# Kernel tuning notes

Measured on AMD Instinct MI355X. Metric: run time of the kernel, lower is better.

Reference implementation:

```python
import jax, jax.numpy as jnp
import numpy as np

N = 50000   # nodes per graph
D = 256     # embedding dim
E = 800000  # edges per graph
NEG_SLOPE = 0.2
EPS = 1e-9


def gat_layer(h, src, dst, W, a):
    # SpGraphAttentionLayer: transform, edge attention exp(-leakyrelu(a.[h_i||h_j])),
    # softmax-normalized scatter aggregation, ELU activation.
    h = h @ W                                   # [N, D]
    # a.[h_src || h_dst] == (h @ a[:D])[src] + (h @ a[D:])[dst]  (avoids [E,2D] concat)
    alpha_src = h @ a[:D]                       # [N]
    alpha_dst = h @ a[D:]                       # [N]
    logits = alpha_src[src] + alpha_dst[dst]    # [E]
    e = jnp.exp(-jax.nn.leaky_relu(logits, NEG_SLOPE))  # [E], pyGAT sparse form
    rowsum = jax.ops.segment_sum(e, src, num_segments=N)            # [N]
    num = jax.ops.segment_sum(e[:, None] * h[dst], src, num_segments=N)  # [N, D]
    out = num / (rowsum[:, None] + EPS)
    return jax.nn.elu(out)


def setup_inputs() -> dict:
    key = jax.random.key(0)
    ks = jax.random.split(key, 8)
    w_std = float(np.sqrt(2.0 / (D + D)))  # xavier
    sr_emb = jax.random.normal(ks[0], (N, D), jnp.float32) * w_std
    tg_emb = jax.random.normal(ks[1], (N, D), jnp.float32) * w_std
    W1 = jax.random.normal(ks[2], (D, D), jnp.float32) * w_std
    a1 = jax.random.normal(ks[3], (2 * D,), jnp.float32) * 0.1
    W2 = jax.random.normal(ks[4], (D, D), jnp.float32) * w_std
    a2 = jax.random.normal(ks[5], (2 * D,), jnp.float32) * 0.1
    adj_sr = jax.random.randint(ks[6], (2, E), 0, N, dtype=jnp.int64)
    adj_tg = jax.random.randint(ks[7], (2, E), 0, N, dtype=jnp.int64)
    return {"sr_emb": sr_emb, "tg_emb": tg_emb, "W1": W1, "a1": a1,
            "W2": W2, "a2": a2, "adj_sr": adj_sr, "adj_tg": adj_tg}


def reference(sr_emb, tg_emb, W1, a1, W2, a2, adj_sr, adj_tg):
    # layers are shared across the two graphs (same ModuleList applied to both)
    src_s, dst_s = adj_sr[0], adj_sr[1]
    src_t, dst_t = adj_tg[0], adj_tg[1]
    for (W, a) in ((W1, a1), (W2, a2)):
        sr_emb = gat_layer(sr_emb, src_s, dst_s, W, a)
        tg_emb = gat_layer(tg_emb, src_t, dst_t, W, a)
    return (sr_emb, tg_emb)
```

## Files before the change

### kernel.cpp

```cpp
#include <hip/hip_runtime.h>

#define NEG_SLOPE 0.2f
#define EPS_ 1e-9f

typedef __attribute__((ext_vector_type(8))) short short8v;
typedef __attribute__((ext_vector_type(4))) float f32x4;

__device__ __forceinline__ float bf2f(unsigned short u) {
    return __uint_as_float(((unsigned)u) << 16);
}
__device__ __forceinline__ unsigned short f2bf(float f) {
    unsigned u = __float_as_uint(f);
    u = u + 0x7FFFu + ((u >> 16) & 1u);
    return (unsigned short)(u >> 16);
}

__global__ void hist_kernel(const int* __restrict__ src, int* __restrict__ cnt, int E) {
    int i = blockIdx.x * blockDim.x + threadIdx.x;
    if (i < E) atomicAdd(&cnt[src[i]], 1);
}

__global__ __launch_bounds__(256) void scan1_kernel(const int* __restrict__ cnt,
        int* __restrict__ locpre, int* __restrict__ blocksum, int n) {
    int t = threadIdx.x;
    int lane = t & 63, wid = t >> 6;
    int base = blockIdx.x * 1024 + t * 4;
    int4 v = {0, 0, 0, 0};
    if (base + 3 < n) {
        v = *(const int4*)(cnt + base);
    } else {
        if (base + 0 < n) v.x = cnt[base + 0];
        if (base + 1 < n) v.y = cnt[base + 1];
        if (base + 2 < n) v.z = cnt[base + 2];
        if (base + 3 < n) v.w = cnt[base + 3];
    }
    int s = v.x + v.y + v.z + v.w;
    int incl = s;
    for (int off = 1; off < 64; off <<= 1) {
        int u = __shfl_up(incl, off);
        if (lane >= off) incl += u;
    }
    __shared__ int ws[4];
    if (lane == 63) ws[wid] = incl;
    __syncthreads();
    int woff = 0;
    for (int i = 0; i < wid; ++i) woff += ws[i];
    int excl = incl - s + woff;
    int4 o;
    o.x = excl; o.y = excl + v.x; o.z = o.y + v.y; o.w = o.z + v.z;
    if (base + 3 < n) {
        *(int4*)(locpre + base) = o;
    } else {
        if (base + 0 < n) locpre[base + 0] = o.x;
        if (base + 1 < n) locpre[base + 1] = o.y;
        if (base + 2 < n) locpre[base + 2] = o.z;
        if (base + 3 < n) locpre[base + 3] = o.w;
    }
    if (t == 255) blocksum[blockIdx.x] = excl + s;
}

__global__ __launch_bounds__(64) void scan2_kernel(int* __restrict__ blocksum, int nb) {
    int lane = threadIdx.x;
    int carry = 0;
    for (int base = 0; base < nb; base += 64) {
        int v = (base + lane < nb) ? blocksum[base + lane] : 0;
        int incl = v;
        for (int off = 1; off < 64; off <<= 1) {
            int u = __shfl_up(incl, off);
            if (lane >= off) incl += u;
        }
        int tot = __shfl(incl, 63);
        if (base + lane < nb) blocksum[base + lane] = incl - v + carry;
        carry += tot;
    }
}

__global__ __launch_bounds__(256) void scan3_kernel(const int* __restrict__ locpre,
        const int* __restrict__ blocksum, int* __restrict__ row_ptr,
        int* __restrict__ cursor, int n, int total) {
    int base = blockIdx.x * 1024 + threadIdx.x * 4;
    int off = blocksum[blockIdx.x];
    if (base + 3 < n) {
        int4 v = *(const int4*)(locpre + base);
        v.x += off; v.y += off; v.z += off; v.w += off;
        *(int4*)(row_ptr + base) = v;
        *(int4*)(cursor + base) = v;
    } else {
        for (int i = 0; i < 4; ++i) {
            if (base + i < n) {
                int v = locpre[base + i] + off;
                row_ptr[base + i] = v;
                cursor[base + i] = v;
            }
        }
    }
    if (blockIdx.x == 0 && threadIdx.x == 0) row_ptr[n] = total;
}

__global__ void scatter_kernel(const int* __restrict__ src, const int* __restrict__ dst,
        int* __restrict__ cursor, int* __restrict__ colv, int E) {
    int i = blockIdx.x * blockDim.x + threadIdx.x;
    if (i < E) {
        int p = atomicAdd(&cursor[src[i]], 1);
        colv[p] = dst[i];
    }
}

__global__ void wt_kernel(const float* __restrict__ W, short* __restrict__ Wt) {
    int nn = blockIdx.x, k = threadIdx.x;
    Wt[nn * 256 + k] = (short)f2bf(W[k * 256 + nn]);
}

template<bool IN_BF16>
__global__ __launch_bounds__(256) void gemm_kernel(const void* __restrict__ hin,
        const short* __restrict__ Wt, short* __restrict__ hp,
        const float* __restrict__ af, float* __restrict__ asrc,
        float* __restrict__ adst, int M) {
    __shared__ short As[64 * 40];
    __shared__ short Bt[256 * 40];
    int tid = threadIdx.x;
    int lane = tid & 63, w = tid >> 6;
    int m0 = blockIdx.x * 64;

    f32x4 acc[16];
#pragma unroll
    for (int t = 0; t < 16; ++t) acc[t] = (f32x4){0.f, 0.f, 0.f, 0.f};

    int ar = tid >> 2;
    int ac = (tid & 3) * 8;
    int agrow = m0 + ar;

    for (int kk = 0; kk < 256; kk += 32) {
        short8v av = (short8v){0,0,0,0,0,0,0,0};
        if constexpr (IN_BF16) {
            if (agrow < M)
                av = *(const short8v*)((const short*)hin + (size_t)agrow * 256 + kk + ac);
        } else {
            if (agrow < M) {
                const float* s = (const float*)hin + (size_t)agrow * 256 + kk + ac;
                float4 v0 = *(const float4*)s;
                float4 v1 = *(const float4*)(s + 4);
                av[0] = (short)f2bf(v0.x); av[1] = (short)f2bf(v0.y);
                av[2] = (short)f2bf(v0.z); av[3] = (short)f2bf(v0.w);
                av[4] = (short)f2bf(v1.x); av[5] = (short)f2bf(v1.y);
                av[6] = (short)f2bf(v1.z); av[7] = (short)f2bf(v1.w);
            }
        }
        *(short8v*)&As[ar * 40 + ac] = av;
        {
            const short* s = Wt + (size_t)tid * 256 + kk;
#pragma unroll
            for (int i = 0; i < 4; ++i)
                *(short8v*)&Bt[tid * 40 + i * 8] = *(const short8v*)(s + i * 8);
        }
        __syncthreads();
        short8v a = *(const short8v*)&As[(16 * w + (lane & 15)) * 40 + (lane >> 4) * 8];
#pragma unroll
        for (int t = 0; t < 16; ++t) {
            short8v b = *(const short8v*)&Bt[(16 * t + (lane & 15)) * 40 + (lane >> 4) * 8];
            acc[t] = __builtin_amdgcn_mfma_f32_16x16x32_bf16(a, b, acc[t], 0, 0, 0);
        }
        __syncthreads();
    }
    int r0 = 16 * w + (lane >> 4) * 4;
    int c0 = lane & 15;
    float a_s[16], a_d[16];
#pragma unroll
    for (int t = 0; t < 16; ++t) {
        a_s[t] = af[16 * t + c0];
        a_d[t] = af[256 + 16 * t + c0];
    }
#pragma unroll
    for (int j = 0; j < 4; ++j) {
        int grow = m0 + r0 + j;
        float ssrc = 0.f, sdst = 0.f;
#pragma unroll
        for (int t = 0; t < 16; ++t) {
            float cv = acc[t][j];
            ssrc = fmaf(cv, a_s[t], ssrc);
            sdst = fmaf(cv, a_d[t], sdst);
            if (grow < M) hp[(size_t)grow * 256 + 16 * t + c0] = (short)f2bf(cv);
        }
        for (int off = 1; off < 16; off <<= 1) {
            ssrc += __shfl_xor(ssrc, off);
            sdst += __shfl_xor(sdst, off);
        }
        if (c0 == 0 && grow < M) { asrc[grow] = ssrc; adst[grow] = sdst; }
    }
}

template<bool OUT_BF16>
__global__ __launch_bounds__(256) void aggregate_kernel(const int* __restrict__ row_ptr,
        const int* __restrict__ colv, const float* __restrict__ asrc,
        const float* __restrict__ adst, const unsigned short* __restrict__ hp,
        void* __restrict__ outp, int n) {
    int node = (blockIdx.x * blockDim.x + threadIdx.x) >> 6;
    int lane = threadIdx.x & 63;
    if (node >= n) return;
    node = __builtin_amdgcn_readfirstlane(node);
    int beg = row_ptr[node], end = row_ptr[node + 1];
    float ai = asrc[node];
    const ushort4* __restrict__ hpv = (const ushort4*)hp;
    float acc0 = 0.f, acc1 = 0.f, acc2 = 0.f, acc3 = 0.f, rs = 0.f;
    for (int e = beg; e < end; e += 16) {
        int m = end - e;
        int js[16]; float ds[16]; ushort4 qs[16];
#pragma unroll
        for (int k = 0; k < 16; ++k)
            if (k < m) { js[k] = colv[e + k]; ds[k] = adst[js[k]]; }
#pragma unroll
        for (int k = 0; k < 16; ++k)
            if (k < m) qs[k] = hpv[(size_t)js[k] * 64 + lane];
#pragma unroll
        for (int k = 0; k < 16; ++k)
            if (k < m) {
                float x = ai + ds[k];
                float lr = fmaxf(x, NEG_SLOPE * x);
                float wk = __expf(-lr);
                ushort4 q = qs[k];
                acc0 = fmaf(wk, bf2f(q.x), acc0);
                acc1 = fmaf(wk, bf2f(q.y), acc1);
                acc2 = fmaf(wk, bf2f(q.z), acc2);
                acc3 = fmaf(wk, bf2f(q.w), acc3);
                rs += wk;
            }
    }
    float inv = 1.f / (rs + EPS_);
    float v0 = acc0 * inv, v1 = acc1 * inv, v2 = acc2 * inv, v3 = acc3 * inv;
    v0 = v0 > 0.f ? v0 : __expf(v0) - 1.f;
    v1 = v1 > 0.f ? v1 : __expf(v1) - 1.f;
    v2 = v2 > 0.f ? v2 : __expf(v2) - 1.f;
    v3 = v3 > 0.f ? v3 : __expf(v3) - 1.f;
    if constexpr (OUT_BF16) {
        ushort4 o;
        o.x = f2bf(v0); o.y = f2bf(v1); o.z = f2bf(v2); o.w = f2bf(v3);
        *(ushort4*)((unsigned short*)outp + (size_t)node * 256 + lane * 4) = o;
    } else {
        float4 o = {v0, v1, v2, v3};
        *(float4*)((float*)outp + (size_t)node * 256 + lane * 4) = o;
    }
}

extern "C" void kernel_launch(void* const* d_in, const int* in_sizes, int n_in,
                              void* d_out, int out_size, void* d_ws, size_t ws_size,
                              hipStream_t stream) {
    const float* sr_emb = (const float*)d_in[0];
    const float* tg_emb = (const float*)d_in[1];
    const float* W1 = (const float*)d_in[2];
    const float* a1 = (const float*)d_in[3];
    const float* W2 = (const float*)d_in[4];
    const float* a2 = (const float*)d_in[5];
    const int* adj_sr = (const int*)d_in[6];
    const int* adj_tg = (const int*)d_in[7];
    int N = in_sizes[0] / 256;
    int E = in_sizes[6] / 2;

    char* p = (char*)d_ws;
    auto alloc = [&](size_t bytes) -> void* {
        void* r = (void*)p;
        p += (bytes + 255) & ~(size_t)255;
        return r;
    };
    int nb = (N + 1023) / 1024;
    int* cnt      = (int*)alloc((size_t)N * 4);
    int* row_ptr  = (int*)alloc((size_t)(N + 1) * 4);
    int* cursor   = (int*)alloc((size_t)N * 4);
    int* locpre   = (int*)alloc((size_t)N * 4);
    int* blocksum = (int*)alloc((size_t)nb * 4);
    int* colv     = (int*)alloc((size_t)E * 4);
    short* Wt1    = (short*)alloc(256 * 256 * 2);
    short* Wt2    = (short*)alloc(256 * 256 * 2);
    short* hp     = (short*)alloc((size_t)N * 256 * 2);
    float* asrc   = (float*)alloc((size_t)N * 4);
    float* adst   = (float*)alloc((size_t)N * 4);
    short* tmp    = (short*)alloc((size_t)N * 256 * 2);

    wt_kernel<<<256, 256, 0, stream>>>(W1, Wt1);
    wt_kernel<<<256, 256, 0, stream>>>(W2, Wt2);

    int gemm_grid = (N + 63) / 64;
    int nw_grid = (N + 3) / 4;
    int e_grid = (E + 255) / 256;

    for (int g = 0; g < 2; ++g) {
        const int* srcv = (g == 0 ? adj_sr : adj_tg);
        const int* dstv = srcv + E;
        const float* emb = (g == 0 ? sr_emb : tg_emb);
        float* outg = (float*)d_out + (size_t)g * N * 256;

        hipMemsetAsync(cnt, 0, (size_t)N * 4, stream);
        hist_kernel<<<e_grid, 256, 0, stream>>>(srcv, cnt, E);
        scan1_kernel<<<nb, 256, 0, stream>>>(cnt, locpre, blocksum, N);
        scan2_kernel<<<1, 64, 0, stream>>>(blocksum, nb);
        scan3_kernel<<<nb, 256, 0, stream>>>(locpre, blocksum, row_ptr, cursor, N, E);
        scatter_kernel<<<e_grid, 256, 0, stream>>>(srcv, dstv, cursor, colv, E);

        gemm_kernel<false><<<gemm_grid, 256, 0, stream>>>(emb, Wt1, hp, a1, asrc, adst, N);
        aggregate_kernel<true><<<nw_grid, 256, 0, stream>>>(row_ptr, colv, asrc, adst,
                (const unsigned short*)hp, tmp, N);
        gemm_kernel<true><<<gemm_grid, 256, 0, stream>>>(tmp, Wt2, hp, a2, asrc, adst, N);
        aggregate_kernel<false><<<nw_grid, 256, 0, stream>>>(row_ptr, colv, asrc, adst,
                (const unsigned short*)hp, outg, N);
    }
}
```

Baseline: 716.4 us.

## Precompute edge attention weights in a separate kernel and vectorize aggregation loads

```diff
diff --git a/kernel.cpp b/kernel.cpp
--- a/kernel.cpp
+++ b/kernel.cpp
@@ -98,11 +98,24 @@
 }
 
 __global__ void scatter_kernel(const int* __restrict__ src, const int* __restrict__ dst,
-        int* __restrict__ cursor, int* __restrict__ colv, int E) {
+        int* __restrict__ cursor, int* __restrict__ colv, int* __restrict__ srce, int E) {
     int i = blockIdx.x * blockDim.x + threadIdx.x;
     if (i < E) {
-        int p = atomicAdd(&cursor[src[i]], 1);
+        int s = src[i];
+        int p = atomicAdd(&cursor[s], 1);
         colv[p] = dst[i];
+        srce[p] = s;
+    }
+}
+
+__global__ __launch_bounds__(256) void ew_kernel(const int* __restrict__ srce,
+        const int* __restrict__ colv, const float* __restrict__ asrc,
+        const float* __restrict__ adst, float* __restrict__ ew, int E) {
+    int i = blockIdx.x * blockDim.x + threadIdx.x;
+    if (i < E) {
+        float x = asrc[srce[i]] + adst[colv[i]];
+        float lr = fmaxf(x, NEG_SLOPE * x);
+        ew[i] = __expf(-lr);
     }
 }
 
@@ -189,41 +202,71 @@
     }
 }
 
+#define GATH(qq, jj) qq = hpv[(size_t)(jj) * 64 + lane];
+#define CONS(qq, ww) { acc0 = fmaf(ww, bf2f(qq.x), acc0); acc1 = fmaf(ww, bf2f(qq.y), acc1); \
+                       acc2 = fmaf(ww, bf2f(qq.z), acc2); acc3 = fmaf(ww, bf2f(qq.w), acc3); \
+                       rs += ww; }
+
 template<bool OUT_BF16>
 __global__ __launch_bounds__(256) void aggregate_kernel(const int* __restrict__ row_ptr,
-        const int* __restrict__ colv, const float* __restrict__ asrc,
-        const float* __restrict__ adst, const unsigned short* __restrict__ hp,
-        void* __restrict__ outp, int n) {
+        const int* __restrict__ colv, const float* __restrict__ ew,
+        const unsigned short* __restrict__ hp, void* __restrict__ outp, int n) {
     int node = (blockIdx.x * blockDim.x + threadIdx.x) >> 6;
     int lane = threadIdx.x & 63;
     if (node >= n) return;
-    node = __builtin_amdgcn_readfirstlane(node);
     int beg = row_ptr[node], end = row_ptr[node + 1];
-    float ai = asrc[node];
     const ushort4* __restrict__ hpv = (const ushort4*)hp;
     float acc0 = 0.f, acc1 = 0.f, acc2 = 0.f, acc3 = 0.f, rs = 0.f;
-    for (int e = beg; e < end; e += 16) {
+    int e = beg;
+    for (; e + 16 <= end; e += 16) {
+        int4 j0 = *(const int4*)(colv + e);
+        int4 j1 = *(const int4*)(colv + e + 4);
+        int4 j2 = *(const int4*)(colv + e + 8);
+        int4 j3 = *(const int4*)(colv + e + 12);
+        float4 w0 = *(const float4*)(ew + e);
+        float4 w1 = *(const float4*)(ew + e + 4);
+        float4 w2 = *(const float4*)(ew + e + 8);
+        float4 w3 = *(const float4*)(ew + e + 12);
+        ushort4 q0, q1, q2, q3, q4, q5, q6, q7, q8, q9, qa, qb, qc, qd, qe, qf;
+        GATH(q0, j0.x) GATH(q1, j0.y) GATH(q2, j0.z) GATH(q3, j0.w)
+        GATH(q4, j1.x) GATH(q5, j1.y) GATH(q6, j1.z) GATH(q7, j1.w)
+        GATH(q8, j2.x) GATH(q9, j2.y) GATH(qa, j2.z) GATH(qb, j2.w)
+        GATH(qc, j3.x) GATH(qd, j3.y) GATH(qe, j3.z) GATH(qf, j3.w)
+        CONS(q0, w0.x) CONS(q1, w0.y) CONS(q2, w0.z) CONS(q3, w0.w)
+        CONS(q4, w1.x) CONS(q5, w1.y) CONS(q6, w1.z) CONS(q7, w1.w)
+        CONS(q8, w2.x) CONS(q9, w2.y) CONS(qa, w2.z) CONS(qb, w2.w)
+        CONS(qc, w3.x) CONS(qd, w3.y) CONS(qe, w3.z) CONS(qf, w3.w)
+    }
+    if (e < end) {
         int m = end - e;
-        int js[16]; float ds[16]; ushort4 qs[16];
-#pragma unroll
-        for (int k = 0; k < 16; ++k)
-            if (k < m) { js[k] = colv[e + k]; ds[k] = adst[js[k]]; }
-#pragma unroll
-        for (int k = 0; k < 16; ++k)
-            if (k < m) qs[k] = hpv[(size_t)js[k] * 64 + lane];
-#pragma unroll
-        for (int k = 0; k < 16; ++k)
-            if (k < m) {
-                float x = ai + ds[k];
-                float lr = fmaxf(x, NEG_SLOPE * x);
-                float wk = __expf(-lr);
-                ushort4 q = qs[k];
-                acc0 = fmaf(wk, bf2f(q.x), acc0);
-                acc1 = fmaf(wk, bf2f(q.y), acc1);
-                acc2 = fmaf(wk, bf2f(q.z), acc2);
-                acc3 = fmaf(wk, bf2f(q.w), acc3);
-                rs += wk;
-            }
+        int4 j0 = *(const int4*)(colv + e);
+        int4 j1 = *(const int4*)(colv + e + 4);
+        int4 j2 = *(const int4*)(colv + e + 8);
+        int4 j3 = *(const int4*)(colv + e + 12);
+        float4 w0 = *(const float4*)(ew + e);
+        float4 w1 = *(const float4*)(ew + e + 4);
+        float4 w2 = *(const float4*)(ew + e + 8);
+        float4 w3 = *(const float4*)(ew + e + 12);
+        ushort4 q0, q1, q2, q3, q4, q5, q6, q7, q8, q9, qa, qb, qc, qd, qe, qf;
+        GATH(q0, j0.x) GATH(q1, j0.y) GATH(q2, j0.z) GATH(q3, j0.w)
+        GATH(q4, j1.x) GATH(q5, j1.y) GATH(q6, j1.z) GATH(q7, j1.w)
+        GATH(q8, j2.x) GATH(q9, j2.y) GATH(qa, j2.z) GATH(qb, j2.w)
+        GATH(qc, j3.x) GATH(qd, j3.y) GATH(qe, j3.z) GATH(qf, j3.w)
+        CONS(q0, w0.x)
+        if (m > 1)  CONS(q1, w0.y)
+        if (m > 2)  CONS(q2, w0.z)
+        if (m > 3)  CONS(q3, w0.w)
+        if (m > 4)  CONS(q4, w1.x)
+        if (m > 5)  CONS(q5, w1.y)
+        if (m > 6)  CONS(q6, w1.z)
+        if (m > 7)  CONS(q7, w1.w)
+        if (m > 8)  CONS(q8, w2.x)
+        if (m > 9)  CONS(q9, w2.y)
+        if (m > 10) CONS(qa, w2.z)
+        if (m > 11) CONS(qb, w2.w)
+        if (m > 12) CONS(qc, w3.x)
+        if (m > 13) CONS(qd, w3.y)
+        if (m > 14) CONS(qe, w3.z)
     }
     float inv = 1.f / (rs + EPS_);
     float v0 = acc0 * inv, v1 = acc1 * inv, v2 = acc2 * inv, v3 = acc3 * inv;
@@ -267,7 +310,9 @@
     int* cursor   = (int*)alloc((size_t)N * 4);
     int* locpre   = (int*)alloc((size_t)N * 4);
     int* blocksum = (int*)alloc((size_t)nb * 4);
-    int* colv     = (int*)alloc((size_t)E * 4);
+    int* colv     = (int*)alloc((size_t)(E + 16) * 4);
+    int* srce     = (int*)alloc((size_t)E * 4);
+    float* ew     = (float*)alloc((size_t)(E + 16) * 4);
     short* Wt1    = (short*)alloc(256 * 256 * 2);
     short* Wt2    = (short*)alloc(256 * 256 * 2);
     short* hp     = (short*)alloc((size_t)N * 256 * 2);
@@ -289,17 +334,20 @@
         float* outg = (float*)d_out + (size_t)g * N * 256;
 
         hipMemsetAsync(cnt, 0, (size_t)N * 4, stream);
+        hipMemsetAsync(colv + E, 0, 16 * 4, stream);
         hist_kernel<<<e_grid, 256, 0, stream>>>(srcv, cnt, E);
         scan1_kernel<<<nb, 256, 0, stream>>>(cnt, locpre, blocksum, N);
         scan2_kernel<<<1, 64, 0, stream>>>(blocksum, nb);
         scan3_kernel<<<nb, 256, 0, stream>>>(locpre, blocksum, row_ptr, cursor, N, E);
-        scatter_kernel<<<e_grid, 256, 0, stream>>>(srcv, dstv, cursor, colv, E);
+        scatter_kernel<<<e_grid, 256, 0, stream>>>(srcv, dstv, cursor, colv, srce, E);
 
         gemm_kernel<false><<<gemm_grid, 256, 0, stream>>>(emb, Wt1, hp, a1, asrc, adst, N);
-        aggregate_kernel<true><<<nw_grid, 256, 0, stream>>>(row_ptr, colv, asrc, adst,
+        ew_kernel<<<e_grid, 256, 0, stream>>>(srce, colv, asrc, adst, ew, E);
+        aggregate_kernel<true><<<nw_grid, 256, 0, stream>>>(row_ptr, colv, ew,
                 (const unsigned short*)hp, tmp, N);
         gemm_kernel<true><<<gemm_grid, 256, 0, stream>>>(tmp, Wt2, hp, a2, asrc, adst, N);
-        aggregate_kernel<false><<<nw_grid, 256, 0, stream>>>(row_ptr, colv, asrc, adst,
+        ew_kernel<<<e_grid, 256, 0, stream>>>(srce, colv, asrc, adst, ew, E);
+        aggregate_kernel<false><<<nw_grid, 256, 0, stream>>>(row_ptr, colv, ew,
                 (const unsigned short*)hp, outg, N);
     }
 }
```

After: 636.6 us. 11.1% less time.

## Slice features into 32-column planes and precompute per-edge weights for aggregation

Applied to the files above, without the earlier changes.

```diff
diff --git a/kernel.cpp b/kernel.cpp
--- a/kernel.cpp
+++ b/kernel.cpp
@@ -34,6 +34,7 @@
         if (base + 2 < n) v.z = cnt[base + 2];
         if (base + 3 < n) v.w = cnt[base + 3];
     }
+    v.x += v.x & 1; v.y += v.y & 1; v.z += v.z & 1; v.w += v.w & 1;
     int s = v.x + v.y + v.z + v.w;
     int incl = s;
     for (int off = 1; off < 64; off <<= 1) {
@@ -59,7 +60,8 @@
     if (t == 255) blocksum[blockIdx.x] = excl + s;
 }
 
-__global__ __launch_bounds__(64) void scan2_kernel(int* __restrict__ blocksum, int nb) {
+__global__ __launch_bounds__(64) void scan2_kernel(int* __restrict__ blocksum, int nb,
+        int* __restrict__ totout) {
     int lane = threadIdx.x;
     int carry = 0;
     for (int base = 0; base < nb; base += 64) {
@@ -73,11 +75,12 @@
         if (base + lane < nb) blocksum[base + lane] = incl - v + carry;
         carry += tot;
     }
+    if (lane == 0) *totout = carry;
 }
 
 __global__ __launch_bounds__(256) void scan3_kernel(const int* __restrict__ locpre,
         const int* __restrict__ blocksum, int* __restrict__ row_ptr,
-        int* __restrict__ cursor, int n, int total) {
+        int* __restrict__ cursor, int n) {
     int base = blockIdx.x * 1024 + threadIdx.x * 4;
     int off = blocksum[blockIdx.x];
     if (base + 3 < n) {
@@ -94,15 +97,39 @@
             }
         }
     }
-    if (blockIdx.x == 0 && threadIdx.x == 0) row_ptr[n] = total;
 }
 
 __global__ void scatter_kernel(const int* __restrict__ src, const int* __restrict__ dst,
-        int* __restrict__ cursor, int* __restrict__ colv, int E) {
+        int* __restrict__ cursor, int* __restrict__ colv, int* __restrict__ srce, int E) {
     int i = blockIdx.x * blockDim.x + threadIdx.x;
     if (i < E) {
-        int p = atomicAdd(&cursor[src[i]], 1);
+        int s = src[i];
+        int p = atomicAdd(&cursor[s], 1);
         colv[p] = dst[i];
+        srce[p] = s;
+    }
+}
+
+__global__ __launch_bounds__(256) void ew_kernel(const int* __restrict__ srce,
+        const int* __restrict__ colv, const float* __restrict__ asrc,
+        const float* __restrict__ adst, int2* __restrict__ ewc,
+        const int* __restrict__ ptot_p, int n) {
+    int i = blockIdx.x * blockDim.x + threadIdx.x;
+    if (i >= *ptot_p) return;
+    int s = min(max(srce[i], 0), n - 1);
+    int d = min(max(colv[i], 0), n - 1);
+    float x = asrc[s] + adst[d];
+    float lr = fmaxf(x, NEG_SLOPE * x);
+    float w = __expf(-lr);
+    ewc[i] = make_int2(d, __float_as_int(w));
+}
+
+__global__ __launch_bounds__(256) void padfill_kernel(const int* __restrict__ cursor,
+        const int* __restrict__ row_ptr, int2* __restrict__ ewc, int n) {
+    int v = blockIdx.x * blockDim.x + threadIdx.x;
+    if (v < n) {
+        int e = row_ptr[v + 1];
+        for (int p = cursor[v]; p < e; ++p) ewc[p] = make_int2(0, 0);
     }
 }
 
@@ -113,7 +140,7 @@
 
 template<bool IN_BF16>
 __global__ __launch_bounds__(256) void gemm_kernel(const void* __restrict__ hin,
-        const short* __restrict__ Wt, short* __restrict__ hp,
+        const short* __restrict__ Wt, unsigned short* __restrict__ hpS,
         const float* __restrict__ af, float* __restrict__ asrc,
         float* __restrict__ adst, int M) {
     __shared__ short As[64 * 40];
@@ -121,6 +148,7 @@
     int tid = threadIdx.x;
     int lane = tid & 63, w = tid >> 6;
     int m0 = blockIdx.x * 64;
+    size_t Ns = (size_t)M * 32;
 
     f32x4 acc[16];
 #pragma unroll
@@ -179,7 +207,9 @@
             float cv = acc[t][j];
             ssrc = fmaf(cv, a_s[t], ssrc);
             sdst = fmaf(cv, a_d[t], sdst);
-            if (grow < M) hp[(size_t)grow * 256 + 16 * t + c0] = (short)f2bf(cv);
+            int col = 16 * t + c0;
+            if (grow < M)
+                hpS[(size_t)(col >> 5) * Ns + (size_t)grow * 32 + (col & 31)] = f2bf(cv);
         }
         for (int off = 1; off < 16; off <<= 1) {
             ssrc += __shfl_xor(ssrc, off);
@@ -191,53 +221,52 @@
 
 template<bool OUT_BF16>
 __global__ __launch_bounds__(256) void aggregate_kernel(const int* __restrict__ row_ptr,
-        const int* __restrict__ colv, const float* __restrict__ asrc,
-        const float* __restrict__ adst, const unsigned short* __restrict__ hp,
+        const int2* __restrict__ ewc, const unsigned short* __restrict__ hpS,
         void* __restrict__ outp, int n) {
-    int node = (blockIdx.x * blockDim.x + threadIdx.x) >> 6;
+    int bid = blockIdx.x;
+    int slice = bid & 7;
+    int node = (bid >> 3) * 4 + (threadIdx.x >> 6);
     int lane = threadIdx.x & 63;
     if (node >= n) return;
-    node = __builtin_amdgcn_readfirstlane(node);
     int beg = row_ptr[node], end = row_ptr[node + 1];
-    float ai = asrc[node];
-    const ushort4* __restrict__ hpv = (const ushort4*)hp;
-    float acc0 = 0.f, acc1 = 0.f, acc2 = 0.f, acc3 = 0.f, rs = 0.f;
-    for (int e = beg; e < end; e += 16) {
-        int m = end - e;
-        int js[16]; float ds[16]; ushort4 qs[16];
-#pragma unroll
-        for (int k = 0; k < 16; ++k)
-            if (k < m) { js[k] = colv[e + k]; ds[k] = adst[js[k]]; }
-#pragma unroll
-        for (int k = 0; k < 16; ++k)
-            if (k < m) qs[k] = hpv[(size_t)js[k] * 64 + lane];
-#pragma unroll
-        for (int k = 0; k < 16; ++k)
-            if (k < m) {
-                float x = ai + ds[k];
-                float lr = fmaxf(x, NEG_SLOPE * x);
-                float wk = __expf(-lr);
-                ushort4 q = qs[k];
-                acc0 = fmaf(wk, bf2f(q.x), acc0);
-                acc1 = fmaf(wk, bf2f(q.y), acc1);
-                acc2 = fmaf(wk, bf2f(q.z), acc2);
-                acc3 = fmaf(wk, bf2f(q.w), acc3);
-                rs += wk;
-            }
-    }
-    float inv = 1.f / (rs + EPS_);
-    float v0 = acc0 * inv, v1 = acc1 * inv, v2 = acc2 * inv, v3 = acc3 * inv;
-    v0 = v0 > 0.f ? v0 : __expf(v0) - 1.f;
-    v1 = v1 > 0.f ? v1 : __expf(v1) - 1.f;
-    v2 = v2 > 0.f ? v2 : __expf(v2) - 1.f;
-    v3 = v3 > 0.f ? v3 : __expf(v3) - 1.f;
-    if constexpr (OUT_BF16) {
-        ushort4 o;
-        o.x = f2bf(v0); o.y = f2bf(v1); o.z = f2bf(v2); o.w = f2bf(v3);
-        *(ushort4*)((unsigned short*)outp + (size_t)node * 256 + lane * 4) = o;
-    } else {
-        float4 o = {v0, v1, v2, v3};
-        *(float4*)((float*)outp + (size_t)node * 256 + lane * 4) = o;
+    const unsigned short* __restrict__ base = hpS + (size_t)slice * ((size_t)n * 32);
+    int c = lane & 31;
+    int hi = lane >> 5;
+    float acc = 0.f, rs = 0.f;
+    int e = beg;
+    for (; e + 8 <= end; e += 8) {
+        int4 p0 = *(const int4*)(ewc + e);
+        int4 p1 = *(const int4*)(ewc + e + 2);
+        int4 p2 = *(const int4*)(ewc + e + 4);
+        int4 p3 = *(const int4*)(ewc + e + 6);
+        int j0 = hi ? p0.z : p0.x; float w0 = __int_as_float(hi ? p0.w : p0.y);
+        int j1 = hi ? p1.z : p1.x; float w1 = __int_as_float(hi ? p1.w : p1.y);
+        int j2 = hi ? p2.z : p2.x; float w2 = __int_as_float(hi ? p2.w : p2.y);
+        int j3 = hi ? p3.z : p3.x; float w3 = __int_as_float(hi ? p3.w : p3.y);
+        unsigned short q0 = base[(unsigned)j0 * 32 + c];
+        unsigned short q1 = base[(unsigned)j1 * 32 + c];
+        unsigned short q2 = base[(unsigned)j2 * 32 + c];
+        unsigned short q3 = base[(unsigned)j3 * 32 + c];
+        acc = fmaf(w0, bf2f(q0), acc); rs += w0;
+        acc = fmaf(w1, bf2f(q1), acc); rs += w1;
+        acc = fmaf(w2, bf2f(q2), acc); rs += w2;
+        acc = fmaf(w3, bf2f(q3), acc); rs += w3;
+    }
+    for (; e < end; e += 2) {
+        int4 p0 = *(const int4*)(ewc + e);
+        int j0 = hi ? p0.z : p0.x; float w0 = __int_as_float(hi ? p0.w : p0.y);
+        unsigned short q0 = base[(unsigned)j0 * 32 + c];
+        acc = fmaf(w0, bf2f(q0), acc); rs += w0;
+    }
+    acc += __shfl_xor(acc, 32);
+    rs  += __shfl_xor(rs, 32);
+    if (hi == 0) {
+        float v = acc / (rs + EPS_);
+        v = v > 0.f ? v : __expf(v) - 1.f;
+        if constexpr (OUT_BF16)
+            ((unsigned short*)outp)[(size_t)node * 256 + slice * 32 + c] = f2bf(v);
+        else
+            ((float*)outp)[(size_t)node * 256 + slice * 32 + c] = v;
     }
 }
 
@@ -262,15 +291,18 @@
         return r;
     };
     int nb = (N + 1023) / 1024;
+    int EP = E + N + 16;
     int* cnt      = (int*)alloc((size_t)N * 4);
     int* row_ptr  = (int*)alloc((size_t)(N + 1) * 4);
     int* cursor   = (int*)alloc((size_t)N * 4);
     int* locpre   = (int*)alloc((size_t)N * 4);
     int* blocksum = (int*)alloc((size_t)nb * 4);
-    int* colv     = (int*)alloc((size_t)E * 4);
+    int* colv     = (int*)alloc((size_t)EP * 4);
+    int* srce     = (int*)alloc((size_t)EP * 4);
+    int2* ewc     = (int2*)alloc((size_t)EP * 8);
     short* Wt1    = (short*)alloc(256 * 256 * 2);
     short* Wt2    = (short*)alloc(256 * 256 * 2);
-    short* hp     = (short*)alloc((size_t)N * 256 * 2);
+    unsigned short* hpS = (unsigned short*)alloc((size_t)N * 256 * 2);
     float* asrc   = (float*)alloc((size_t)N * 4);
     float* adst   = (float*)alloc((size_t)N * 4);
     short* tmp    = (short*)alloc((size_t)N * 256 * 2);
@@ -279,8 +311,10 @@
     wt_kernel<<<256, 256, 0, stream>>>(W2, Wt2);
 
     int gemm_grid = (N + 63) / 64;
-    int nw_grid = (N + 3) / 4;
+    int agg_grid = 8 * ((N + 3) / 4);
     int e_grid = (E + 255) / 256;
+    int ep_grid = (EP + 255) / 256;
+    int n_grid = (N + 255) / 256;
 
     for (int g = 0; g < 2; ++g) {
         const int* srcv = (g == 0 ? adj_sr : adj_tg);
@@ -291,15 +325,17 @@
         hipMemsetAsync(cnt, 0, (size_t)N * 4, stream);
         hist_kernel<<<e_grid, 256, 0, stream>>>(srcv, cnt, E);
         scan1_kernel<<<nb, 256, 0, stream>>>(cnt, locpre, blocksum, N);
-        scan2_kernel<<<1, 64, 0, stream>>>(blocksum, nb);
-        scan3_kernel<<<nb, 256, 0, stream>>>(locpre, blocksum, row_ptr, cursor, N, E);
-        scatter_kernel<<<e_grid, 256, 0, stream>>>(srcv, dstv, cursor, colv, E);
-
-        gemm_kernel<false><<<gemm_grid, 256, 0, stream>>>(emb, Wt1, hp, a1, asrc, adst, N);
-        aggregate_kernel<true><<<nw_grid, 256, 0, stream>>>(row_ptr, colv, asrc, adst,
-                (const unsigned short*)hp, tmp, N);
-        gemm_kernel<true><<<gemm_grid, 256, 0, stream>>>(tmp, Wt2, hp, a2, asrc, adst, N);
-        aggregate_kernel<false><<<nw_grid, 256, 0, stream>>>(row_ptr, colv, asrc, adst,
-                (const unsigned short*)hp, outg, N);
-    }
-}
+        scan2_kernel<<<1, 64, 0, stream>>>(blocksum, nb, row_ptr + N);
+        scan3_kernel<<<nb, 256, 0, stream>>>(locpre, blocksum, row_ptr, cursor, N);
+        scatter_kernel<<<e_grid, 256, 0, stream>>>(srcv, dstv, cursor, colv, srce, E);
+
+        gemm_kernel<false><<<gemm_grid, 256, 0, stream>>>(emb, Wt1, hpS, a1, asrc, adst, N);
+        ew_kernel<<<ep_grid, 256, 0, stream>>>(srce, colv, asrc, adst, ewc, row_ptr + N, N);
+        padfill_kernel<<<n_grid, 256, 0, stream>>>(cursor, row_ptr, ewc, N);
+        aggregate_kernel<true><<<agg_grid, 256, 0, stream>>>(row_ptr, ewc, hpS, tmp, N);
+        gemm_kernel<true><<<gemm_grid, 256, 0, stream>>>(tmp, Wt2, hpS, a2, asrc, adst, N);
+        ew_kernel<<<ep_grid, 256, 0, stream>>>(srce, colv, asrc, adst, ewc, row_ptr + N, N);
+        padfill_kernel<<<n_grid, 256, 0, stream>>>(cursor, row_ptr, ewc, N);
+        aggregate_kernel<false><<<agg_grid, 256, 0, stream>>>(row_ptr, ewc, hpS, outg, N);
+    }
+}
```

After: 1.049 ms. 1.46x slower.
